# Kernel tuning notes

Measured on AMD Instinct MI355X. Metric: run time of the kernel, lower is better.

## Reference

```python
import jax, jax.numpy as jnp
import numpy as np

B, N, H = 8, 256, 128
EDGE_IN = 2 * H + 1
NODE_IN = 2 * H


def _glorot(key, shape):
    fan_in, fan_out = shape[0], shape[1]
    lim = 1.0 / np.sqrt(fan_in)
    return jax.random.uniform(key, shape, jnp.float32, -lim, lim)


def setup_inputs() -> dict:
    key = jax.random.key(0)
    ks = jax.random.split(key, 12)
    node_state = jax.random.normal(ks[0], (B, N, H), jnp.float32)
    positions = jax.random.normal(ks[1], (B, N, 3), jnp.float32)
    mask = jnp.ones((B, N), jnp.float32)
    # edge_mlp: Linear(2H+1 -> H), SiLU, Linear(H -> H)  (weights stored [in, out])
    We1 = _glorot(ks[2], (EDGE_IN, H)); be1 = _glorot(ks[3], (1, H))[0]
    We2 = _glorot(ks[4], (H, H));       be2 = _glorot(ks[5], (1, H))[0]
    # node_mlp: Linear(2H -> H), SiLU, Linear(H -> H)
    Wn1 = _glorot(ks[6], (NODE_IN, H)); bn1 = _glorot(ks[7], (1, H))[0]
    Wn2 = _glorot(ks[8], (H, H));       bn2 = _glorot(ks[9], (1, H))[0]
    return {"node_state": node_state, "positions": positions, "mask": mask,
            "We1": We1, "be1": be1, "We2": We2, "be2": be2,
            "Wn1": Wn1, "bn1": bn1, "Wn2": Wn2, "bn2": bn2}


def reference(node_state, positions, mask, We1, be1, We2, be2, Wn1, bn1, Wn2, bn2):
    b, n, h = node_state.shape
    # pairwise distances [B, N, N, 1]; safe-sqrt so grad at i==j is 0 (exact fwd)
    rel = positions[:, :, None, :] - positions[:, None, :, :]
    sq = jnp.sum(rel * rel, axis=-1, keepdims=True)
    dist = jnp.where(sq > 0, jnp.sqrt(jnp.where(sq > 0, sq, 1.0)), 0.0)
    # broadcast-concat node features for all pairs -> [B, N, N, 2H+1]
    node_i = jnp.broadcast_to(node_state[:, :, None, :], (b, n, n, h))
    node_j = jnp.broadcast_to(node_state[:, None, :, :], (b, n, n, h))
    edge_input = jnp.concatenate([node_i, node_j, dist], axis=-1)
    edge_msg = jax.nn.silu(edge_input @ We1 + be1) @ We2 + be2  # [B,N,N,H]
    # pairwise validity mask [B, N, N, 1]
    edge_mask = (mask[:, None, :] * mask[:, :, None])[..., None]
    edge_msg = edge_msg * edge_mask
    # masked mean over j
    denom = jnp.clip(jnp.sum(edge_mask, axis=2), 1.0, None)  # [B,N,1]
    aggregated = jnp.sum(edge_msg, axis=2) / denom           # [B,N,H]
    node_in = jnp.concatenate([node_state, aggregated], axis=-1)
    updated = jax.nn.silu(node_in @ Wn1 + bn1) @ Wn2 + bn2
    return node_state + updated * mask[..., None]
```

## Files before the change

### kernel.cpp

```cpp
#include <hip/hip_runtime.h>
#include <math.h>

#define B_ 8
#define N_ 256
#define H_ 128
#define NODES_ (B_ * N_)

#define LOG2E 1.442695041f
#define LN2   0.6931471806f

__device__ __forceinline__ float silu_fast(float x) {
    float e = __expf(-x);
    return x * __builtin_amdgcn_rcpf(1.0f + e);
}

__device__ __forceinline__ void splitk_gemm(
    const float* __restrict__ Wb,
    const float (*actm)[128],
    float (*pls)[4][128], int kseg, int c0)
{
    float4 w[8];
    #pragma unroll
    for (int u = 0; u < 8; ++u) w[u] = *(const float4*)(Wb + u * H_);
    #pragma unroll
    for (int n = 0; n < 4; ++n) {
        float vv[8];
        *(float4*)(vv)     = *(const float4*)(&actm[n][kseg * 8]);
        *(float4*)(vv + 4) = *(const float4*)(&actm[n][kseg * 8 + 4]);
        float4 a = {0.f, 0.f, 0.f, 0.f};
        #pragma unroll
        for (int u = 0; u < 8; ++u) {
            a.x = fmaf(vv[u], w[u].x, a.x);
            a.y = fmaf(vv[u], w[u].y, a.y);
            a.z = fmaf(vv[u], w[u].z, a.z);
            a.w = fmaf(vv[u], w[u].w, a.w);
        }
        *(float4*)(&pls[kseg][n][c0]) = a;
    }
}

__global__ __launch_bounds__(512) void k1q(
    const float* __restrict__ node, const float* __restrict__ We1,
    const float* __restrict__ mask, float* __restrict__ Q)
{
    __shared__ __align__(16) float act[4][128];
    __shared__ __align__(16) float pls[16][4][128];
    const int t = threadIdx.x;
    const int node0 = blockIdx.x * 4;

    if (t < 128) {
        int r = t >> 5, col = (t & 31) * 4;
        *(float4*)(&act[r][col]) = *(const float4*)(node + (size_t)(node0 + r) * H_ + col);
    }
    const int kseg = t >> 5;
    const int c0   = (t & 31) * 4;
    __syncthreads();

    splitk_gemm(We1 + (size_t)(128 + kseg * 8) * H_ + c0, act, pls, kseg, c0);
    __syncthreads();
    {
        const int n = t >> 7, c = t & 127;
        float s = 0.f;
        #pragma unroll
        for (int seg = 0; seg < 16; ++seg) s += pls[seg][n][c];
        const float m = mask[node0 + n];
        Q[(size_t)(node0 + n) * H_ + c] = fmaf(-LOG2E, s, (1.0f - m) * 1e30f);
    }
}

__global__ __launch_bounds__(512) void k2(
    const float* __restrict__ Qv, const float* __restrict__ We1,
    const float* __restrict__ be1, const float* __restrict__ positions,
    const float* __restrict__ mask, const float* __restrict__ node,
    const float* __restrict__ We2, const float* __restrict__ be2,
    const float* __restrict__ Wn1, const float* __restrict__ bn1,
    const float* __restrict__ Wn2, const float* __restrict__ bn2,
    float* __restrict__ out)
{
    __shared__ __align__(16) float arena[8192];
    __shared__ __align__(16) float dls[256][4];
    __shared__ __align__(16) float Sls[4][128];
    __shared__ __align__(16) float Tls[4][128];
    __shared__ __align__(16) float Pls[4][128];
    __shared__ __align__(16) float prels[4][128];
    __shared__ float cs;

    const int t  = threadIdx.x;
    const int b  = blockIdx.x >> 6;
    const int i0 = (blockIdx.x & 63) * 4;
    const int node0 = b * N_ + i0;

    const float4* __restrict__ Qg = (const float4*)(Qv + (size_t)(b * N_) * H_);
    float4 r0 = Qg[0 * 512 + t];
    float4 r1 = Qg[1 * 512 + t];
    float4 r2 = Qg[2 * 512 + t];
    float4 r3 = Qg[3 * 512 + t];

    {
        const int t2 = t & 255;
        const int half = t >> 8;
        const int il = t2 & 3;
        const int jb = t2 >> 2;
        const float* pb = positions + b * N_ * 3;
        const float pix = pb[(i0 + il) * 3 + 0];
        const float piy = pb[(i0 + il) * 3 + 1];
        const float piz = pb[(i0 + il) * 3 + 2];
        #pragma unroll
        for (int s = 0; s < 2; ++s) {
            int j = jb + 64 * (half * 2 + s);
            float dx = pix - pb[j * 3 + 0];
            float dy = piy - pb[j * 3 + 1];
            float dz = piz - pb[j * 3 + 2];
            float sq = dx * dx + dy * dy + dz * dz;
            dls[j][il] = (sq > 0.f) ? sqrtf(sq) : 0.f;
        }
    }
    if (t < 64) {
        float mv = mask[b * N_ + t] + mask[b * N_ + 64 + t]
                 + mask[b * N_ + 128 + t] + mask[b * N_ + 192 + t];
        #pragma unroll
        for (int off = 32; off >= 1; off >>= 1) mv += __shfl_down(mv, off);
        if (t == 0) cs = mv;
    }

    const int kseg = t >> 5;
    const int c0   = (t & 31) * 4;
    float (*pls)[4][128] = (float (*)[4][128])arena;

    if (t < 128) {
        int r = t >> 5, col = (t & 31) * 4;
        *(float4*)(&Tls[r][col]) = *(const float4*)(node + (size_t)(node0 + r) * H_ + col);
    }
    __syncthreads();
    splitk_gemm(We1 + (size_t)(kseg * 8) * H_ + c0, Tls, pls, kseg, c0);
    __syncthreads();
    {
        const int n = t >> 7, c = t & 127;
        float s = 0.f;
        #pragma unroll
        for (int seg = 0; seg < 16; ++seg) s += pls[seg][n][c];
        Pls[n][c] = -LOG2E * (s + be1[c]);
    }
    __syncthreads();
    splitk_gemm(Wn1 + (size_t)(kseg * 8) * H_ + c0, Tls, pls, kseg, c0);
    __syncthreads();
    {
        const int n = t >> 7, c = t & 127;
        float s = 0.f;
        #pragma unroll
        for (int seg = 0; seg < 16; ++seg) s += pls[seg][n][c];
        prels[n][c] = s + bn1[c];
    }

    const int i   = t >> 7;
    const int jq  = (t >> 5) & 3;
    const int cg  = t & 31;
    const int c0e = cg * 4;

    float4 wd4 = *(const float4*)(We1 + (size_t)256 * H_ + c0e);
    wd4.x *= -LOG2E; wd4.y *= -LOG2E; wd4.z *= -LOG2E; wd4.w *= -LOG2E;
    const float4 base4 = *(const float4*)(&Pls[i][c0e]);
    float4 acc = {0.f, 0.f, 0.f, 0.f};

    for (int ch = 0; ch < 4; ++ch) {
        __syncthreads();
        ((float4*)arena)[0 * 512 + t] = r0;
        ((float4*)arena)[1 * 512 + t] = r1;
        ((float4*)arena)[2 * 512 + t] = r2;
        ((float4*)arena)[3 * 512 + t] = r3;
        if (ch < 3) {
            r0 = Qg[(ch + 1) * 2048 + 0 * 512 + t];
            r1 = Qg[(ch + 1) * 2048 + 1 * 512 + t];
            r2 = Qg[(ch + 1) * 2048 + 2 * 512 + t];
            r3 = Qg[(ch + 1) * 2048 + 3 * 512 + t];
        }
        __syncthreads();
        const float4* qrow = ((const float4*)arena) + (jq * 16) * 32 + cg;
        const int jd = ch * 64 + jq * 16;
        #pragma unroll 8
        for (int jj = 0; jj < 16; ++jj) {
            float4 q = qrow[jj * 32];
            float d  = dls[jd + jj][i];
            float nx = fmaf(d, wd4.x, base4.x + q.x);
            float ny = fmaf(d, wd4.y, base4.y + q.y);
            float nz = fmaf(d, wd4.z, base4.z + q.z);
            float nw = fmaf(d, wd4.w, base4.w + q.w);
            float ex = __builtin_amdgcn_exp2f(nx);
            float ey = __builtin_amdgcn_exp2f(ny);
            float ez = __builtin_amdgcn_exp2f(nz);
            float ew = __builtin_amdgcn_exp2f(nw);
            acc.x = fmaf(nx, __builtin_amdgcn_rcpf(1.0f + ex), acc.x);
            acc.y = fmaf(ny, __builtin_amdgcn_rcpf(1.0f + ey), acc.y);
            acc.z = fmaf(nz, __builtin_amdgcn_rcpf(1.0f + ez), acc.z);
            acc.w = fmaf(nw, __builtin_amdgcn_rcpf(1.0f + ew), acc.w);
        }
    }

    __syncthreads();
    {
        float (*pq)[4][128] = (float (*)[4][128])arena;
        *(float4*)(&pq[jq][i][c0e]) = acc;
    }
    __syncthreads();
    const float mi = mask[node0 + i];
    {
        const int c = t & 127;
        float (*pq)[4][128] = (float (*)[4][128])arena;
        float s = pq[0][i][c] + pq[1][i][c] + pq[2][i][c] + pq[3][i][c];
        const float inv_cnt = __builtin_amdgcn_rcpf(fmaxf(cs, 1.0f));
        Sls[i][c] = (mi * inv_cnt * -LN2) * s;
    }
    __syncthreads();

    splitk_gemm(We2 + (size_t)(kseg * 8) * H_ + c0, Sls, pls, kseg, c0);
    __syncthreads();
    {
        const int c = t & 127;
        float s = 0.f;
        #pragma unroll
        for (int seg = 0; seg < 16; ++seg) s += pls[seg][i][c];
        Tls[i][c] = fmaf(mi, be2[c], s);
    }
    __syncthreads();

    splitk_gemm(Wn1 + (size_t)(128 + kseg * 8) * H_ + c0, Tls, pls, kseg, c0);
    __syncthreads();
    {
        const int c = t & 127;
        float s = 0.f;
        #pragma unroll
        for (int seg = 0; seg < 16; ++seg) s += pls[seg][i][c];
        Sls[i][c] = silu_fast(prels[i][c] + s);
    }
    __syncthreads();

    splitk_gemm(Wn2 + (size_t)(kseg * 8) * H_ + c0, Sls, pls, kseg, c0);
    __syncthreads();
    {
        const int c = t & 127;
        float s = 0.f;
        #pragma unroll
        for (int seg = 0; seg < 16; ++seg) s += pls[seg][i][c];
        const size_t idx = (size_t)(node0 + i) * H_ + c;
        out[idx] = node[idx] + mi * (s + bn2[c]);
    }
}

extern "C" void kernel_launch(void* const* d_in, const int* in_sizes, int n_in,
                              void* d_out, int out_size, void* d_ws, size_t ws_size,
                              hipStream_t stream)
{
    const float* node      = (const float*)d_in[0];
    const float* positions = (const float*)d_in[1];
    const float* mask      = (const float*)d_in[2];
    const float* We1       = (const float*)d_in[3];
    const float* be1       = (const float*)d_in[4];
    const float* We2       = (const float*)d_in[5];
    const float* be2       = (const float*)d_in[6];
    const float* Wn1       = (const float*)d_in[7];
    const float* bn1       = (const float*)d_in[8];
    const float* Wn2       = (const float*)d_in[9];
    const float* bn2       = (const float*)d_in[10];
    float* out = (float*)d_out;

    float* Q = (float*)d_ws;

    k1q<<<512, 512, 0, stream>>>(node, We1, mask, Q);
    k2 <<<512, 512, 0, stream>>>(Q, We1, be1, positions, mask, node,
                                 We2, be2, Wn1, bn1, Wn2, bn2, out);
}
```

Measured before the change: 101.4 us.

## Read Q rows directly from global and compute all four nodes per thread

```diff
diff --git a/kernel.cpp b/kernel.cpp
--- a/kernel.cpp
+++ b/kernel.cpp
@@ -90,12 +90,6 @@
     const int i0 = (blockIdx.x & 63) * 4;
     const int node0 = b * N_ + i0;
 
-    const float4* __restrict__ Qg = (const float4*)(Qv + (size_t)(b * N_) * H_);
-    float4 r0 = Qg[0 * 512 + t];
-    float4 r1 = Qg[1 * 512 + t];
-    float4 r2 = Qg[2 * 512 + t];
-    float4 r3 = Qg[3 * 512 + t];
-
     {
         const int t2 = t & 255;
         const int half = t >> 8;
@@ -151,62 +145,60 @@
         for (int seg = 0; seg < 16; ++seg) s += pls[seg][n][c];
         prels[n][c] = s + bn1[c];
     }
-
-    const int i   = t >> 7;
-    const int jq  = (t >> 5) & 3;
+    __syncthreads();
+
+    const int jh  = t >> 5;
     const int cg  = t & 31;
     const int c0e = cg * 4;
 
     float4 wd4 = *(const float4*)(We1 + (size_t)256 * H_ + c0e);
     wd4.x *= -LOG2E; wd4.y *= -LOG2E; wd4.z *= -LOG2E; wd4.w *= -LOG2E;
-    const float4 base4 = *(const float4*)(&Pls[i][c0e]);
-    float4 acc = {0.f, 0.f, 0.f, 0.f};
-
-    for (int ch = 0; ch < 4; ++ch) {
-        __syncthreads();
-        ((float4*)arena)[0 * 512 + t] = r0;
-        ((float4*)arena)[1 * 512 + t] = r1;
-        ((float4*)arena)[2 * 512 + t] = r2;
-        ((float4*)arena)[3 * 512 + t] = r3;
-        if (ch < 3) {
-            r0 = Qg[(ch + 1) * 2048 + 0 * 512 + t];
-            r1 = Qg[(ch + 1) * 2048 + 1 * 512 + t];
-            r2 = Qg[(ch + 1) * 2048 + 2 * 512 + t];
-            r3 = Qg[(ch + 1) * 2048 + 3 * 512 + t];
+
+    float4 bse[4];
+    #pragma unroll
+    for (int i2 = 0; i2 < 4; ++i2)
+        bse[i2] = *(const float4*)(&Pls[i2][c0e]);
+
+    float4 acc[4];
+    #pragma unroll
+    for (int i2 = 0; i2 < 4; ++i2) acc[i2] = make_float4(0.f, 0.f, 0.f, 0.f);
+
+    const float4* __restrict__ Qg4 = (const float4*)(Qv + (size_t)(b * N_) * H_);
+
+    #pragma unroll 4
+    for (int jl = 0; jl < 16; ++jl) {
+        const int j = jh * 16 + jl;
+        const float4 q  = Qg4[j * 32 + cg];
+        const float4 d4 = *(const float4*)(&dls[j][0]);
+        const float dd[4] = {d4.x, d4.y, d4.z, d4.w};
+        #pragma unroll
+        for (int i2 = 0; i2 < 4; ++i2) {
+            float nx = fmaf(dd[i2], wd4.x, bse[i2].x + q.x);
+            float ny = fmaf(dd[i2], wd4.y, bse[i2].y + q.y);
+            float nz = fmaf(dd[i2], wd4.z, bse[i2].z + q.z);
+            float nw = fmaf(dd[i2], wd4.w, bse[i2].w + q.w);
+            acc[i2].x = fmaf(nx, __builtin_amdgcn_rcpf(1.0f + __builtin_amdgcn_exp2f(nx)), acc[i2].x);
+            acc[i2].y = fmaf(ny, __builtin_amdgcn_rcpf(1.0f + __builtin_amdgcn_exp2f(ny)), acc[i2].y);
+            acc[i2].z = fmaf(nz, __builtin_amdgcn_rcpf(1.0f + __builtin_amdgcn_exp2f(nz)), acc[i2].z);
+            acc[i2].w = fmaf(nw, __builtin_amdgcn_rcpf(1.0f + __builtin_amdgcn_exp2f(nw)), acc[i2].w);
         }
-        __syncthreads();
-        const float4* qrow = ((const float4*)arena) + (jq * 16) * 32 + cg;
-        const int jd = ch * 64 + jq * 16;
-        #pragma unroll 8
-        for (int jj = 0; jj < 16; ++jj) {
-            float4 q = qrow[jj * 32];
-            float d  = dls[jd + jj][i];
-            float nx = fmaf(d, wd4.x, base4.x + q.x);
-            float ny = fmaf(d, wd4.y, base4.y + q.y);
-            float nz = fmaf(d, wd4.z, base4.z + q.z);
-            float nw = fmaf(d, wd4.w, base4.w + q.w);
-            float ex = __builtin_amdgcn_exp2f(nx);
-            float ey = __builtin_amdgcn_exp2f(ny);
-            float ez = __builtin_amdgcn_exp2f(nz);
-            float ew = __builtin_amdgcn_exp2f(nw);
-            acc.x = fmaf(nx, __builtin_amdgcn_rcpf(1.0f + ex), acc.x);
-            acc.y = fmaf(ny, __builtin_amdgcn_rcpf(1.0f + ey), acc.y);
-            acc.z = fmaf(nz, __builtin_amdgcn_rcpf(1.0f + ez), acc.z);
-            acc.w = fmaf(nw, __builtin_amdgcn_rcpf(1.0f + ew), acc.w);
-        }
-    }
-
-    __syncthreads();
+    }
+
     {
         float (*pq)[4][128] = (float (*)[4][128])arena;
-        *(float4*)(&pq[jq][i][c0e]) = acc;
-    }
-    __syncthreads();
+        #pragma unroll
+        for (int i2 = 0; i2 < 4; ++i2)
+            *(float4*)(&pq[jh][i2][c0e]) = acc[i2];
+    }
+    __syncthreads();
+    const int i = t >> 7;
     const float mi = mask[node0 + i];
     {
         const int c = t & 127;
         float (*pq)[4][128] = (float (*)[4][128])arena;
-        float s = pq[0][i][c] + pq[1][i][c] + pq[2][i][c] + pq[3][i][c];
+        float s = 0.f;
+        #pragma unroll
+        for (int seg = 0; seg < 16; ++seg) s += pq[seg][i][c];
         const float inv_cnt = __builtin_amdgcn_rcpf(fmaxf(cs, 1.0f));
         Sls[i][c] = (mi * inv_cnt * -LN2) * s;
     }
```

Measured after the change: 100.4 us. About the same (-1.1%).
